# Performance work log

Hardware: AMD Instinct MI355X
Metric: run time of the kernel (lower is better)

## Reference

```python
import jax, jax.numpy as jnp
import numpy as np

KH, KW = 3, 3
STRIDE = 1
PADDING = 1
CIN, COUT = 64, 64


def setup_inputs() -> dict:
    key = jax.random.key(0)
    kx, kw, kb = jax.random.split(key, 3)
    x = jax.random.normal(kx, (16, CIN, 112, 112), dtype=jnp.float32)
    # Kaiming-uniform style init, matching the torch module
    fan = CIN * KH * KW
    gain = np.sqrt(2.0)
    bound_w = np.sqrt(3.0) * gain / np.sqrt(fan)
    weights = jax.random.uniform(kw, (COUT, CIN, KH, KW), dtype=jnp.float32,
                                 minval=-bound_w, maxval=bound_w)
    bound_b = 1.0 / np.sqrt(fan)
    bias = jax.random.uniform(kb, (COUT,), dtype=jnp.float32,
                              minval=-bound_b, maxval=bound_b)
    return {"x": x, "weights": weights, "bias": bias}


def reference(x, weights, bias):
    # Equivalent to F.unfold + GEMM: a standard cross-correlation conv.
    # x: (N, C, H, W), weights: (F, C, KH, KW) -> out: (N, F, H', W')
    out = jax.lax.conv_general_dilated(
        x, weights,
        window_strides=(STRIDE, STRIDE),
        padding=((PADDING, PADDING), (PADDING, PADDING)),
        dimension_numbers=("NCHW", "OIHW", "NCHW"),
    )
    return out + bias[None, :, None, None]
```

## Files before the change

kernel.cpp:

```cpp
#include <hip/hip_runtime.h>


typedef __attribute__((ext_vector_type(8))) short bf16x8;
typedef __attribute__((ext_vector_type(4))) float f32x4;

#define CIN 64
#define COUT 64
#define HH 112
#define WW 112
#define ROWS 2
#define DYS  4
#define WCMAX 66
#define PLANE (8 * WCMAX * 8)
#define LDS_SHORTS (DYS * PLANE)

__device__ __forceinline__ int ladr(int dy, int oct, int w) {
    return ((dy * 8 + oct) * WCMAX + w) * 8;
}

__device__ __forceinline__ unsigned short f2bf(float f) {
    unsigned u = __builtin_bit_cast(unsigned, f);
    u += 0x7FFFu + ((u >> 16) & 1u);
    return (unsigned short)(u >> 16);
}

#if __has_builtin(__builtin_amdgcn_cvt_pk_bf16_f32)
__device__ __forceinline__ unsigned pk2bf(float a, float b) {
    typedef __attribute__((ext_vector_type(2))) __bf16 bf16x2;
    bf16x2 r = __builtin_amdgcn_cvt_pk_bf16_f32(a, b);
    return __builtin_bit_cast(unsigned, r);
}
#else
__device__ __forceinline__ unsigned pk2bf(float a, float b) {
    return (unsigned)f2bf(a) | ((unsigned)f2bf(b) << 16);
}
#endif

__global__ void conv_wprep(const float* __restrict__ w, short* __restrict__ wbf) {
    int i = blockIdx.x * 256 + threadIdx.x;
    int j = i & 7;
    int f = (i >> 3) & 63;
    int koct = (i >> 9) & 3;
    int cb = (i >> 11) & 1;
    int t = i >> 12;
    int c = cb * 32 + koct * 8 + j;
    int ky = t / 3, kx = t - ky * 3;
    wbf[i] = (short)f2bf(w[((f * CIN + c) * 3 + ky) * 3 + kx]);
}

template<int MT>
__device__ __forceinline__ void main_loop(const short* lds, const short* __restrict__ wbf,
                                          f32x4 (&acc)[4][2], bf16x8 (&br)[2][2][2],
                                          int r, int nh, int lm, int q)
{
#pragma unroll
    for (int t = 0; t < 9; ++t) {
        const int buf = t & 1;
        if (t < 8) {
#pragma unroll
            for (int ntl = 0; ntl < 2; ++ntl) {
                const int f = (nh * 2 + ntl) * 16 + lm;
                br[1 - buf][ntl][0] = *(const bf16x8*)(wbf + ((t + 1) * 8 + q) * 512 + f * 8);
                br[1 - buf][ntl][1] = *(const bf16x8*)(wbf + ((t + 1) * 8 + 4 + q) * 512 + f * 8);
            }
        }
        const int ky = t / 3, kx = t - ky * 3;
#pragma unroll
        for (int mt = 0; mt < MT; ++mt) {
            const int wcol = mt * 16 + lm + kx;
            const bf16x8 a0 = *(const bf16x8*)&lds[ladr(r + ky, q, wcol)];
            const bf16x8 a1 = *(const bf16x8*)&lds[ladr(r + ky, q + 4, wcol)];
#pragma unroll
            for (int ntl = 0; ntl < 2; ++ntl)
                acc[mt][ntl] = __builtin_amdgcn_mfma_f32_16x16x32_bf16(a0, br[buf][ntl][0], acc[mt][ntl], 0, 0, 0);
#pragma unroll
            for (int ntl = 0; ntl < 2; ++ntl)
                acc[mt][ntl] = __builtin_amdgcn_mfma_f32_16x16x32_bf16(a1, br[buf][ntl][1], acc[mt][ntl], 0, 0, 0);
        }
    }
}

__global__ __launch_bounds__(256, 4)
void conv3x3_mfma(const float* __restrict__ x, const short* __restrict__ wbf,
                  const float* __restrict__ bias, float* __restrict__ out)
{
    __shared__ __align__(16) short lds[LDS_SHORTS];
    const int tid = threadIdx.x;
    const int n = blockIdx.x;
    const int h0 = blockIdx.y * ROWS;
    const int ws = blockIdx.z;
    const int MTN = ws ? 3 : 4;
    const int c0 = ws * 64;

    const int wave = tid >> 6;
    const int r  = wave >> 1;
    const int nh = wave & 1;
    const int lane = tid & 63;
    const int lm = lane & 15;
    const int q  = lane >> 4;

    if (tid < 32) {
        const int dy = tid >> 3, oct = tid & 7;
        const int padw = ws ? 49 : 0;
        *(uint4*)&lds[ladr(dy, oct, padw)] = (uint4){0u, 0u, 0u, 0u};
    }
    if (h0 == 0) {
        uint4* p = (uint4*)&lds[0];
        for (int i = tid; i < PLANE / 8; i += 256) p[i] = (uint4){0u, 0u, 0u, 0u};
    }
    if (h0 == HH - ROWS) {
        uint4* p = (uint4*)&lds[(DYS - 1) * PLANE];
        for (int i = tid; i < PLANE / 8; i += 256) p[i] = (uint4){0u, 0u, 0u, 0u};
    }
    {
        const int W4N = ws ? 12 : 16;
        const int dy = tid >> 6, oct = (tid >> 3) & 7, w4lo = tid & 7;
        const int gh = h0 + dy - 1;
        if ((unsigned)gh < (unsigned)HH) {
            for (int w4 = w4lo; w4 < W4N; w4 += 8) {
                const float* px = x + (((n * CIN + oct * 8) * HH + gh) * WW + c0 + w4 * 4);
                float v[8][4];
#pragma unroll
                for (int k = 0; k < 8; ++k) {
                    const float4 t = *(const float4*)(px + k * HH * WW);
                    v[k][0] = t.x; v[k][1] = t.y; v[k][2] = t.z; v[k][3] = t.w;
                }
#pragma unroll
                for (int dw = 0; dw < 4; ++dw) {
                    uint4 pk;
                    pk.x = pk2bf(v[0][dw], v[1][dw]);
                    pk.y = pk2bf(v[2][dw], v[3][dw]);
                    pk.z = pk2bf(v[4][dw], v[5][dw]);
                    pk.w = pk2bf(v[6][dw], v[7][dw]);
                    *(uint4*)&lds[ladr(dy, oct, 1 + w4 * 4 + dw)] = pk;
                }
            }
        }
    }
    {
        const int dy = tid >> 6, c = tid & 63;
        const int gh = h0 + dy - 1;
        const int gce = ws ? 63 : 64;
        const int wedge = ws ? 0 : 65;
        if ((unsigned)gh < (unsigned)HH) {
            const float vv = x[((n * CIN + c) * HH + gh) * WW + gce];
            lds[ladr(dy, c >> 3, wedge) + (c & 7)] = (short)f2bf(vv);
        }
    }

    bf16x8 br[2][2][2];
#pragma unroll
    for (int ntl = 0; ntl < 2; ++ntl) {
        const int f = (nh * 2 + ntl) * 16 + lm;
        br[0][ntl][0] = *(const bf16x8*)(wbf + (q) * 512 + f * 8);
        br[0][ntl][1] = *(const bf16x8*)(wbf + (4 + q) * 512 + f * 8);
    }

    __syncthreads();

    f32x4 acc[4][2];
#pragma unroll
    for (int mt = 0; mt < 4; ++mt)
#pragma unroll
        for (int ntl = 0; ntl < 2; ++ntl) acc[mt][ntl] = (f32x4){0.f, 0.f, 0.f, 0.f};

    if (MTN == 4) main_loop<4>(lds, wbf, acc, br, r, nh, lm, q);
    else          main_loop<3>(lds, wbf, acc, br, r, nh, lm, q);

    const int f0 = nh * 32 + lm;
    const float b0 = bias[f0];
    const float b1 = bias[f0 + 16];
    const int hrow = h0 + r;
#pragma unroll
    for (int mt = 0; mt < 4; ++mt) {
        if (mt < MTN) {
#pragma unroll
            for (int ntl = 0; ntl < 2; ++ntl) {
                const f32x4 v = acc[mt][ntl];
                const float bb = ntl ? b1 : b0;
                float4 s;
                s.x = v[0] + bb; s.y = v[1] + bb; s.z = v[2] + bb; s.w = v[3] + bb;
                const int f = f0 + ntl * 16;
                *(float4*)(out + ((n * COUT + f) * HH + hrow) * WW + c0 + mt * 16 + q * 4) = s;
            }
        }
    }
}

extern "C" void kernel_launch(void* const* d_in, const int* in_sizes, int n_in,
                              void* d_out, int out_size, void* d_ws, size_t ws_size,
                              hipStream_t stream) {
    const float* x = (const float*)d_in[0];
    const float* w = (const float*)d_in[1];
    const float* b = (const float*)d_in[2];
    float* out = (float*)d_out;
    short* wbf = (short*)d_ws;

    conv_wprep<<<144, 256, 0, stream>>>(w, wbf);
    dim3 grid(16, HH / ROWS, 2);
    conv3x3_mfma<<<grid, 256, 0, stream>>>(x, wbf, b, out);
}
```

Baseline: 125.1 us.

## Make blocks persistent over row strips with rolling LDS ring and prefetch

Each block now walks a 14-row strip in 7 two-row tiles. Input rows sit in an 8-plane LDS ring, so halo rows are loaded once per strip instead of being reloaded for every two-row tile. The next rows are fetched from global memory into registers while the MFMA work runs, and all 9 weight taps stay in registers. The grid shrinks from 1792 blocks to 256 with launch bounds of 1, which cuts occupancy and parallelism and raises register pressure.

```diff
diff --git a/kernel.cpp b/kernel.cpp
--- a/kernel.cpp
+++ b/kernel.cpp
@@ -9,13 +9,15 @@
 #define HH 112
 #define WW 112
 #define ROWS 2
-#define DYS  4
+#define TILES 7
+#define STRIPH (ROWS * TILES)
+#define NPL 8
 #define WCMAX 66
 #define PLANE (8 * WCMAX * 8)
-#define LDS_SHORTS (DYS * PLANE)
-
-__device__ __forceinline__ int ladr(int dy, int oct, int w) {
-    return ((dy * 8 + oct) * WCMAX + w) * 8;
+#define LDS_SHORTS (NPL * PLANE)
+
+__device__ __forceinline__ int ladr(int pl, int oct, int w) {
+    return ((pl * 8 + oct) * WCMAX + w) * 8;
 }
 
 __device__ __forceinline__ unsigned short f2bf(float f) {
@@ -48,49 +50,90 @@
     wbf[i] = (short)f2bf(w[((f * CIN + c) * 3 + ky) * 3 + kx]);
 }
 
-template<int MT>
-__device__ __forceinline__ void main_loop(const short* lds, const short* __restrict__ wbf,
-                                          f32x4 (&acc)[4][2], bf16x8 (&br)[2][2][2],
-                                          int r, int nh, int lm, int q)
+struct StageRegs {
+    float v[8][4];
+    float hv;
+};
+
+__device__ __forceinline__ void stage_load(const float* __restrict__ x, int tid,
+                                           int n, int c0, int W4N, int gce,
+                                           int row0, StageRegs& sr)
 {
-#pragma unroll
-    for (int t = 0; t < 9; ++t) {
-        const int buf = t & 1;
-        if (t < 8) {
-#pragma unroll
-            for (int ntl = 0; ntl < 2; ++ntl) {
-                const int f = (nh * 2 + ntl) * 16 + lm;
-                br[1 - buf][ntl][0] = *(const bf16x8*)(wbf + ((t + 1) * 8 + q) * 512 + f * 8);
-                br[1 - buf][ntl][1] = *(const bf16x8*)(wbf + ((t + 1) * 8 + 4 + q) * 512 + f * 8);
-            }
-        }
-        const int ky = t / 3, kx = t - ky * 3;
-#pragma unroll
-        for (int mt = 0; mt < MT; ++mt) {
-            const int wcol = mt * 16 + lm + kx;
-            const bf16x8 a0 = *(const bf16x8*)&lds[ladr(r + ky, q, wcol)];
-            const bf16x8 a1 = *(const bf16x8*)&lds[ladr(r + ky, q + 4, wcol)];
-#pragma unroll
-            for (int ntl = 0; ntl < 2; ++ntl)
-                acc[mt][ntl] = __builtin_amdgcn_mfma_f32_16x16x32_bf16(a0, br[buf][ntl][0], acc[mt][ntl], 0, 0, 0);
-#pragma unroll
-            for (int ntl = 0; ntl < 2; ++ntl)
-                acc[mt][ntl] = __builtin_amdgcn_mfma_f32_16x16x32_bf16(a1, br[buf][ntl][1], acc[mt][ntl], 0, 0, 0);
-        }
-    }
-}
-
-__global__ __launch_bounds__(256, 4)
+    const int re  = tid >> 7;
+    const int oct = (tid >> 4) & 7;
+    const int w4  = tid & 15;
+    const int row = row0 + re;
+    sr.hv = 0.f;
+#pragma unroll
+    for (int k = 0; k < 8; ++k)
+#pragma unroll
+        for (int d = 0; d < 4; ++d) sr.v[k][d] = 0.f;
+    if ((unsigned)row < (unsigned)HH && w4 < W4N) {
+        const float* px = x + (((n * CIN + oct * 8) * HH + row) * WW + c0 + w4 * 4);
+#pragma unroll
+        for (int k = 0; k < 8; ++k) {
+            const float4 t = *(const float4*)(px + k * HH * WW);
+            sr.v[k][0] = t.x; sr.v[k][1] = t.y; sr.v[k][2] = t.z; sr.v[k][3] = t.w;
+        }
+    }
+    if (tid < 128) {
+        const int hrow = row0 + (tid >> 6);
+        const int c = tid & 63;
+        if ((unsigned)hrow < (unsigned)HH)
+            sr.hv = x[((n * CIN + c) * HH + hrow) * WW + gce];
+    }
+}
+
+__device__ __forceinline__ void stage_write(short* lds, int tid, int W4N,
+                                            int padw, int wedge, int row0,
+                                            const StageRegs& sr)
+{
+    const int re  = tid >> 7;
+    const int oct = (tid >> 4) & 7;
+    const int w4  = tid & 15;
+    const int row = row0 + re;
+    const int pl  = row & (NPL - 1);
+    if (w4 < W4N) {
+#pragma unroll
+        for (int dw = 0; dw < 4; ++dw) {
+            uint4 pk;
+            pk.x = pk2bf(sr.v[0][dw], sr.v[1][dw]);
+            pk.y = pk2bf(sr.v[2][dw], sr.v[3][dw]);
+            pk.z = pk2bf(sr.v[4][dw], sr.v[5][dw]);
+            pk.w = pk2bf(sr.v[6][dw], sr.v[7][dw]);
+            *(uint4*)&lds[ladr(pl, oct, 1 + w4 * 4 + dw)] = pk;
+        }
+    }
+    if (tid < 128) {
+        const int hrow = row0 + (tid >> 6);
+        const int c = tid & 63;
+        const int hpl = hrow & (NPL - 1);
+        lds[ladr(hpl, c >> 3, wedge) + (c & 7)] = (short)f2bf(sr.hv);
+    }
+    if (tid < 16) {
+        const int prow = row0 + (tid >> 3);
+        const int ppl = prow & (NPL - 1);
+        *(uint4*)&lds[ladr(ppl, tid & 7, padw)] = (uint4){0u, 0u, 0u, 0u};
+    }
+}
+
+__global__ __launch_bounds__(256, 1)
 void conv3x3_mfma(const float* __restrict__ x, const short* __restrict__ wbf,
                   const float* __restrict__ bias, float* __restrict__ out)
 {
     __shared__ __align__(16) short lds[LDS_SHORTS];
     const int tid = threadIdx.x;
     const int n = blockIdx.x;
-    const int h0 = blockIdx.y * ROWS;
-    const int ws = blockIdx.z;
-    const int MTN = ws ? 3 : 4;
-    const int c0 = ws * 64;
+    const int ws = blockIdx.y;
+    const int strip = blockIdx.z;
+    const int hb = strip * STRIPH;
+
+    const int MTN  = ws ? 3 : 4;
+    const int W4N  = ws ? 12 : 16;
+    const int c0   = ws * 64;
+    const int padw = ws ? 49 : 0;
+    const int gce  = ws ? 63 : 64;
+    const int wedge = ws ? 0 : 65;
 
     const int wave = tid >> 6;
     const int r  = wave >> 1;
@@ -99,91 +142,78 @@
     const int lm = lane & 15;
     const int q  = lane >> 4;
 
-    if (tid < 32) {
-        const int dy = tid >> 3, oct = tid & 7;
-        const int padw = ws ? 49 : 0;
-        *(uint4*)&lds[ladr(dy, oct, padw)] = (uint4){0u, 0u, 0u, 0u};
-    }
-    if (h0 == 0) {
-        uint4* p = (uint4*)&lds[0];
-        for (int i = tid; i < PLANE / 8; i += 256) p[i] = (uint4){0u, 0u, 0u, 0u};
-    }
-    if (h0 == HH - ROWS) {
-        uint4* p = (uint4*)&lds[(DYS - 1) * PLANE];
-        for (int i = tid; i < PLANE / 8; i += 256) p[i] = (uint4){0u, 0u, 0u, 0u};
-    }
-    {
-        const int W4N = ws ? 12 : 16;
-        const int dy = tid >> 6, oct = (tid >> 3) & 7, w4lo = tid & 7;
-        const int gh = h0 + dy - 1;
-        if ((unsigned)gh < (unsigned)HH) {
-            for (int w4 = w4lo; w4 < W4N; w4 += 8) {
-                const float* px = x + (((n * CIN + oct * 8) * HH + gh) * WW + c0 + w4 * 4);
-                float v[8][4];
-#pragma unroll
-                for (int k = 0; k < 8; ++k) {
-                    const float4 t = *(const float4*)(px + k * HH * WW);
-                    v[k][0] = t.x; v[k][1] = t.y; v[k][2] = t.z; v[k][3] = t.w;
-                }
-#pragma unroll
-                for (int dw = 0; dw < 4; ++dw) {
-                    uint4 pk;
-                    pk.x = pk2bf(v[0][dw], v[1][dw]);
-                    pk.y = pk2bf(v[2][dw], v[3][dw]);
-                    pk.z = pk2bf(v[4][dw], v[5][dw]);
-                    pk.w = pk2bf(v[6][dw], v[7][dw]);
-                    *(uint4*)&lds[ladr(dy, oct, 1 + w4 * 4 + dw)] = pk;
-                }
-            }
-        }
-    }
-    {
-        const int dy = tid >> 6, c = tid & 63;
-        const int gh = h0 + dy - 1;
-        const int gce = ws ? 63 : 64;
-        const int wedge = ws ? 0 : 65;
-        if ((unsigned)gh < (unsigned)HH) {
-            const float vv = x[((n * CIN + c) * HH + gh) * WW + gce];
-            lds[ladr(dy, c >> 3, wedge) + (c & 7)] = (short)f2bf(vv);
-        }
-    }
-
-    bf16x8 br[2][2][2];
-#pragma unroll
-    for (int ntl = 0; ntl < 2; ++ntl) {
-        const int f = (nh * 2 + ntl) * 16 + lm;
-        br[0][ntl][0] = *(const bf16x8*)(wbf + (q) * 512 + f * 8);
-        br[0][ntl][1] = *(const bf16x8*)(wbf + (4 + q) * 512 + f * 8);
-    }
-
-    __syncthreads();
-
-    f32x4 acc[4][2];
-#pragma unroll
-    for (int mt = 0; mt < 4; ++mt)
-#pragma unroll
-        for (int ntl = 0; ntl < 2; ++ntl) acc[mt][ntl] = (f32x4){0.f, 0.f, 0.f, 0.f};
-
-    if (MTN == 4) main_loop<4>(lds, wbf, acc, br, r, nh, lm, q);
-    else          main_loop<3>(lds, wbf, acc, br, r, nh, lm, q);
+    StageRegs sr;
+
+    stage_load(x, tid, n, c0, W4N, gce, hb - 1, sr);
+    stage_write(lds, tid, W4N, padw, wedge, hb - 1, sr);
+    stage_load(x, tid, n, c0, W4N, gce, hb + 1, sr);
+    stage_write(lds, tid, W4N, padw, wedge, hb + 1, sr);
+
+    bf16x8 bw[9][2][2];
+#pragma unroll
+    for (int t = 0; t < 9; ++t)
+#pragma unroll
+        for (int ntl = 0; ntl < 2; ++ntl) {
+            const int f = (nh * 2 + ntl) * 16 + lm;
+            bw[t][ntl][0] = *(const bf16x8*)(wbf + (t * 8 + q) * 512 + f * 8);
+            bw[t][ntl][1] = *(const bf16x8*)(wbf + (t * 8 + 4 + q) * 512 + f * 8);
+        }
 
     const int f0 = nh * 32 + lm;
     const float b0 = bias[f0];
     const float b1 = bias[f0 + 16];
-    const int hrow = h0 + r;
-#pragma unroll
-    for (int mt = 0; mt < 4; ++mt) {
-        if (mt < MTN) {
-#pragma unroll
-            for (int ntl = 0; ntl < 2; ++ntl) {
-                const f32x4 v = acc[mt][ntl];
-                const float bb = ntl ? b1 : b0;
-                float4 s;
-                s.x = v[0] + bb; s.y = v[1] + bb; s.z = v[2] + bb; s.w = v[3] + bb;
-                const int f = f0 + ntl * 16;
-                *(float4*)(out + ((n * COUT + f) * HH + hrow) * WW + c0 + mt * 16 + q * 4) = s;
+
+    __syncthreads();
+
+    for (int t = 0; t < TILES; ++t) {
+        const int h0 = hb + 2 * t;
+        const bool do_stage = (t < TILES - 1);
+
+        if (do_stage) stage_load(x, tid, n, c0, W4N, gce, h0 + 3, sr);
+
+        f32x4 acc[4][2];
+#pragma unroll
+        for (int mt = 0; mt < 4; ++mt)
+#pragma unroll
+            for (int ntl = 0; ntl < 2; ++ntl) acc[mt][ntl] = (f32x4){0.f, 0.f, 0.f, 0.f};
+
+#pragma unroll
+        for (int tap = 0; tap < 9; ++tap) {
+            const int ky = tap / 3, kx = tap - ky * 3;
+            const int pl = (h0 - 1 + r + ky) & (NPL - 1);
+#pragma unroll
+            for (int mt = 0; mt < 4; ++mt) {
+                if (mt < MTN) {
+                    const int wcol = mt * 16 + lm + kx;
+                    const bf16x8 a0 = *(const bf16x8*)&lds[ladr(pl, q, wcol)];
+                    const bf16x8 a1 = *(const bf16x8*)&lds[ladr(pl, q + 4, wcol)];
+                    acc[mt][0] = __builtin_amdgcn_mfma_f32_16x16x32_bf16(a0, bw[tap][0][0], acc[mt][0], 0, 0, 0);
+                    acc[mt][1] = __builtin_amdgcn_mfma_f32_16x16x32_bf16(a0, bw[tap][1][0], acc[mt][1], 0, 0, 0);
+                    acc[mt][0] = __builtin_amdgcn_mfma_f32_16x16x32_bf16(a1, bw[tap][0][1], acc[mt][0], 0, 0, 0);
+                    acc[mt][1] = __builtin_amdgcn_mfma_f32_16x16x32_bf16(a1, bw[tap][1][1], acc[mt][1], 0, 0, 0);
+                }
             }
         }
+
+        if (do_stage) stage_write(lds, tid, W4N, padw, wedge, h0 + 3, sr);
+
+        const int hrow = h0 + r;
+#pragma unroll
+        for (int mt = 0; mt < 4; ++mt) {
+            if (mt < MTN) {
+#pragma unroll
+                for (int ntl = 0; ntl < 2; ++ntl) {
+                    const f32x4 v = acc[mt][ntl];
+                    const float bb = ntl ? b1 : b0;
+                    float4 s;
+                    s.x = v[0] + bb; s.y = v[1] + bb; s.z = v[2] + bb; s.w = v[3] + bb;
+                    *(float4*)(out + ((n * COUT + f0 + ntl * 16) * HH + hrow) * WW
+                               + c0 + mt * 16 + q * 4) = s;
+                }
+            }
+        }
+
+        __syncthreads();
     }
 }
 
@@ -197,6 +227,6 @@
     short* wbf = (short*)d_ws;
 
     conv_wprep<<<144, 256, 0, stream>>>(w, wbf);
-    dim3 grid(16, HH / ROWS, 2);
+    dim3 grid(16, 2, 8);
     conv3x3_mfma<<<grid, 256, 0, stream>>>(x, wbf, b, out);
 }
```

Result: no change. 124.1 us (-0.8%).
